# Optimization experiments

Measured on AMD Instinct MI355X. Metric: run time of the kernel, lower is better.

The kernel has to match this reference:

```python
import jax, jax.numpy as jnp
import numpy as np

H = 16      # num_heads
HD = 128    # head_dim = embed_dim // num_heads
BS = 64     # NSA block_size
SEL = 8     # selected blocks per query (block_counts)
WIN = 64    # sliding window (left) size
BASE = 10000.0


def _rope(t):
    # t: [b, n, h, hd]; rotary LRPE (lrpe_type=1)
    n, hd = t.shape[1], t.shape[-1]
    half = hd // 2
    inv = 1.0 / (BASE ** (jnp.arange(half, dtype=jnp.float32) / half))
    th = jnp.arange(n, dtype=jnp.float32)[:, None] * inv[None, :]  # [n, half]
    cos = jnp.cos(th)[None, :, None, :]
    sin = jnp.sin(th)[None, :, None, :]
    t1, t2 = t[..., :half], t[..., half:]
    return jnp.concatenate([t1 * cos - t2 * sin, t1 * sin + t2 * cos], axis=-1)


def _nsa_forward(x, Wq, Wk, Wv, Wg, Wo):
    b, n, d = x.shape
    nb = n // BS
    scale = HD ** -0.5
    q = (x @ Wq).reshape(b, n, H, HD)
    k = (x @ Wk).reshape(b, n, H, HD)
    v = (x @ Wv).reshape(b, n, H, HD)
    g = jax.nn.sigmoid(x @ Wg)                   # [b, n, 3H]
    g_cmp, g_slc, g_swa = jnp.split(g, 3, axis=-1)
    q = _rope(q)
    k = _rope(k)
    idx = jnp.arange(n)

    # --- compression branch: mean-pooled KV blocks, causal over fully-past blocks
    k_cmp = k.reshape(b, nb, BS, H, HD).mean(axis=2)   # [b, nb, h, hd]
    v_cmp = v.reshape(b, nb, BS, H, HD).mean(axis=2)
    s_cmp = jnp.einsum('bnhd,bmhd->bhnm', q, k_cmp) * scale  # [b, h, n, nb]
    blk_end = (jnp.arange(nb) + 1) * BS - 1
    cmp_mask = idx[:, None] >= blk_end[None, :]        # [n, nb]
    p_cmp = jax.nn.softmax(jnp.where(cmp_mask[None, None], s_cmp, -1e30), axis=-1)
    p_cmp = p_cmp * cmp_mask.any(-1)[None, None, :, None]  # zero rows with no valid block
    o_cmp = jnp.einsum('bhnm,bmhd->bnhd', p_cmp, v_cmp)

    # --- selection branch: top-k blocks by compressed scores, current block forced
    cur_blk = jax.nn.one_hot(idx // BS, nb, dtype=jnp.float32)  # [n, nb]
    imp = p_cmp + 2.0 * cur_blk[None, None]
    sel = jax.lax.top_k(imp, SEL)[1]                   # [b, h, n, SEL]
    blk_sel = jax.nn.one_hot(sel, nb).sum(-2) > 0      # [b, h, n, nb]
    causal = idx[:, None] >= idx[None, :]              # [n, n]
    slc_mask = blk_sel[..., idx // BS] & causal[None, None]  # [b, h, n, n]
    s_full = jnp.einsum('bnhd,bmhd->bhnm', q, k) * scale     # [b, h, n, n]
    p_slc = jax.nn.softmax(jnp.where(slc_mask, s_full, -1e30), axis=-1)
    o_slc = jnp.einsum('bhnm,bmhd->bnhd', p_slc, v)

    swa_mask = causal & (idx[:, None] - idx[None, :] <= WIN)
    p_swa = jax.nn.softmax(jnp.where(swa_mask[None, None], s_full, -1e30), axis=-1)
    o_swa = jnp.einsum('bhnm,bmhd->bnhd', p_swa, v)

    o = (o_cmp * g_cmp[..., None] + o_slc * g_slc[..., None]
         + o_swa * g_swa[..., None])                   # [b, n, h, hd]
    return o.reshape(b, n, H * HD) @ Wo


def setup_inputs() -> dict:
    key = jax.random.key(0)
    ks = jax.random.split(key, 6)
    B, N, D = 2, 1024, 2048
    std = 0.02
    return {
        'x': jax.random.normal(ks[0], (B, N, D), jnp.float32),
        'Wq': jax.random.normal(ks[1], (D, H * HD), jnp.float32) * std,
        'Wk': jax.random.normal(ks[2], (D, H * HD), jnp.float32) * std,
        'Wv': jax.random.normal(ks[3], (D, H * HD), jnp.float32) * std,
        'Wg': jax.random.normal(ks[4], (D, 3 * H), jnp.float32) * std,
        'Wo': jax.random.normal(ks[5], (H * HD, D), jnp.float32) * std,
    }


def reference(x, Wq, Wk, Wv, Wg, Wo):
    return _nsa_forward(x, Wq, Wk, Wv, Wg, Wo)
```

## Files before the change

kernel.cpp:

```cpp
#include <hip/hip_runtime.h>
#include <hip/hip_bf16.h>

#define HN   16
#define HDIM 128
#define NSEQ 1024
#define NBLK 16
#define BSZ  64
#define SCALE 0.08838834764831845f
#define QKV_STR 6400
#define KOFS 2048
#define VOFS 4096
#define GOFS 6144

typedef __attribute__((ext_vector_type(8))) short bfrag;
typedef __attribute__((ext_vector_type(4))) float facc;

__device__ __forceinline__ float bf2f(short s) {
  union { unsigned u; float f; } cv;
  cv.u = ((unsigned)(unsigned short)s) << 16;
  return cv.f;
}
__device__ __forceinline__ short f2bf(float f) {
  unsigned u = __float_as_uint(f);
  u = (u + 0x7fff + ((u >> 16) & 1)) >> 16;
  return (short)u;
}

#define ASYNC16(gp, lp)                                                    \
  __builtin_amdgcn_global_load_lds(                                        \
      (const __attribute__((address_space(1))) void*)(gp),                 \
      (__attribute__((address_space(3))) void*)(lp), 16, 0, 0)

#define MFMA16(a, b, c) __builtin_amdgcn_mfma_f32_16x16x32_bf16(a, b, c, 0, 0, 0)

__global__ __launch_bounds__(256) void prep(const float* __restrict__ Wq,
                                            const float* __restrict__ Wk,
                                            const float* __restrict__ Wv,
                                            const float* __restrict__ Wg,
                                            const float* __restrict__ x,
                                            short* __restrict__ w_t,
                                            short* __restrict__ x_bf) {
  __shared__ float tile[32][33];
  const int z = blockIdx.z;
  const int bx = blockIdx.x * 32, by = blockIdx.y * 32;
  const int tx = threadIdx.x & 31, ty = threadIdx.x >> 5;
  if (z == 4) {
#pragma unroll
    for (int i = 0; i < 4; ++i) {
      const int row = by + ty + 8 * i;
      x_bf[(size_t)row * 2048 + bx + tx] = f2bf(x[(size_t)row * 2048 + bx + tx]);
    }
    return;
  }
  if (z == 3) {
    if (blockIdx.x >= 4) return;
#pragma unroll
    for (int i = 0; i < 4; ++i) {
      const int c = bx + tx;
      tile[ty + 8 * i][tx] = (c < 48) ? Wg[(size_t)(by + ty + 8 * i) * 48 + c] : 0.f;
    }
    __syncthreads();
#pragma unroll
    for (int i = 0; i < 4; ++i)
      w_t[(size_t)(GOFS + bx + ty + 8 * i) * 2048 + by + tx] = f2bf(tile[tx][ty + 8 * i]);
    return;
  }
  const float* src = (z == 0) ? Wq : (z == 1) ? Wk : Wv;
#pragma unroll
  for (int i = 0; i < 4; ++i)
    tile[ty + 8 * i][tx] = src[(size_t)(by + ty + 8 * i) * 2048 + bx + tx];
  __syncthreads();
#pragma unroll
  for (int i = 0; i < 4; ++i)
    w_t[(size_t)(z * 2048 + bx + ty + 8 * i) * 2048 + by + tx] = f2bf(tile[tx][ty + 8 * i]);
}

__global__ __launch_bounds__(256) void transpose_cast(const float* __restrict__ src,
                                                      short* __restrict__ dst) {
  __shared__ float tile[32][33];
  const int bx = blockIdx.x * 32, by = blockIdx.y * 32;
  const int tx = threadIdx.x & 31, ty = threadIdx.x >> 5;
#pragma unroll
  for (int i = 0; i < 4; ++i)
    tile[ty + 8 * i][tx] = src[(size_t)(by + ty + 8 * i) * 2048 + bx + tx];
  __syncthreads();
#pragma unroll
  for (int i = 0; i < 4; ++i)
    dst[(size_t)(bx + ty + 8 * i) * 2048 + by + tx] = f2bf(tile[tx][ty + 8 * i]);
}

__global__ __launch_bounds__(512, 1) void gemm256(const short* __restrict__ A,
                                                  const short* __restrict__ Bt,
                                                  short* __restrict__ C,
                                                  int M, int N, int K) {
  __shared__ short lds[2][2][16384];
  const int t = threadIdx.x;
  const int l = t & 63, w = t >> 6;
  const int wm = w >> 2, wn = w & 3;
  const int lm = l & 15, hi = l >> 4;
  const int lanexor = (lm & 7) << 3;
  const int kk0 = (hi * 8) ^ lanexor;
  const int L = blockIdx.x;
  const int row0 = (L & 7) * 256, col0 = (L >> 3) * 256;
  const int nt = K >> 6;

  const int srow = t >> 3;
  const int scol = 8 * ((t & 7) ^ (srow & 7));
  const short* Ab = A + (size_t)(row0 + srow) * K + scol;
  const short* Bb = Bt + (size_t)(col0 + srow) * K + scol;

#define STAGE(mat, srcbase, h, tau, buf)                                     \
  {                                                                          \
    const short* g_ = (srcbase) + (size_t)(h) * 128 * K + (size_t)(tau) * 64;\
    short* d_ = &lds[buf][mat][(h) * 8192 + t * 8];                          \
    ASYNC16(g_, d_);                                                         \
    ASYNC16(g_ + (size_t)64 * K, d_ + 4096);                                 \
  }

  facc acc[8][4] = {};
  bfrag af[8], bf0[4], bf1[4];

  STAGE(0, Ab, 0, 0, 0); STAGE(0, Ab, 1, 0, 0);
  STAGE(1, Bb, 0, 0, 0); STAGE(1, Bb, 1, 0, 0);
  STAGE(1, Bb, 0, 1, 1); STAGE(1, Bb, 1, 1, 1);
  asm volatile("s_waitcnt vmcnt(4)" ::: "memory");
  __builtin_amdgcn_s_barrier();

  for (int tau = 0; tau < nt; ++tau) {
    const int c = tau & 1;
    const int tA = (tau + 1 < nt) ? tau + 1 : nt - 1;
    const int tB = (tau + 2 < nt) ? tau + 2 : nt - 1;

#define DS_A(qm)                                                             \
  _Pragma("unroll") for (int ii = 0; ii < 4; ++ii) {                         \
    const int row_ = wm * 128 + (qm) * 64 + ii * 16 + lm;                    \
    af[ii * 2 + 0] = *(const bfrag*)&lds[c][0][row_ * 64 + kk0];             \
    af[ii * 2 + 1] = *(const bfrag*)&lds[c][0][row_ * 64 + (kk0 ^ 32)];      \
  }
#define DS_B(qn, arr)                                                        \
  _Pragma("unroll") for (int jj = 0; jj < 2; ++jj) {                         \
    const int row_ = wn * 64 + (qn) * 32 + jj * 16 + lm;                     \
    arr[jj * 2 + 0] = *(const bfrag*)&lds[c][1][row_ * 64 + kk0];            \
    arr[jj * 2 + 1] = *(const bfrag*)&lds[c][1][row_ * 64 + (kk0 ^ 32)];     \
  }
#define QUAD(qm, qn, arr)                                                    \
  _Pragma("unroll") for (int ii = 0; ii < 4; ++ii)                           \
  _Pragma("unroll") for (int jj = 0; jj < 2; ++jj) {                         \
    acc[(qm)*4+ii][(qn)*2+jj] = MFMA16(af[ii*2+0], arr[jj*2+0], acc[(qm)*4+ii][(qn)*2+jj]); \
    acc[(qm)*4+ii][(qn)*2+jj] = MFMA16(af[ii*2+1], arr[jj*2+1], acc[(qm)*4+ii][(qn)*2+jj]); \
  }

    DS_A(0); DS_B(0, bf0);
    STAGE(0, Ab, 0, tA, c ^ 1);
    __builtin_amdgcn_s_barrier();
    asm volatile("s_waitcnt lgkmcnt(0)" ::: "memory");
    __builtin_amdgcn_sched_barrier(0);
    __builtin_amdgcn_s_setprio(1);
    QUAD(0, 0, bf0);
    __builtin_amdgcn_s_setprio(0);
    __builtin_amdgcn_s_barrier();

    DS_B(1, bf1);
    STAGE(0, Ab, 1, tA, c ^ 1);
    __builtin_amdgcn_s_barrier();
    asm volatile("s_waitcnt lgkmcnt(0)" ::: "memory");
    __builtin_amdgcn_sched_barrier(0);
    __builtin_amdgcn_s_setprio(1);
    QUAD(0, 1, bf1);
    __builtin_amdgcn_s_setprio(0);
    __builtin_amdgcn_s_barrier();

    DS_A(1);
    STAGE(1, Bb, 0, tB, c);
    __builtin_amdgcn_s_barrier();
    asm volatile("s_waitcnt lgkmcnt(0)" ::: "memory");
    __builtin_amdgcn_sched_barrier(0);
    __builtin_amdgcn_s_setprio(1);
    QUAD(1, 1, bf1);
    __builtin_amdgcn_s_setprio(0);
    __builtin_amdgcn_s_barrier();

    STAGE(1, Bb, 1, tB, c);
    __builtin_amdgcn_s_setprio(1);
    QUAD(1, 0, bf0);
    __builtin_amdgcn_s_setprio(0);
    asm volatile("s_waitcnt vmcnt(4)" ::: "memory");
    __builtin_amdgcn_s_barrier();
  }

#pragma unroll
  for (int i = 0; i < 8; ++i)
#pragma unroll
    for (int j = 0; j < 4; ++j)
#pragma unroll
      for (int rr = 0; rr < 4; ++rr)
        C[(size_t)(row0 + wm * 128 + i * 16 + hi * 4 + rr) * N +
          col0 + wn * 64 + j * 16 + lm] = f2bf(acc[i][j][rr]);
#undef STAGE
#undef DS_A
#undef DS_B
#undef QUAD
}

__device__ __forceinline__ void store_c(float* p, float v) { *p = v; }
__device__ __forceinline__ void store_c(short* p, float v) { *p = f2bf(v); }

template <typename OT>
__global__ __launch_bounds__(256) void gemm_bf16_bt(const short* __restrict__ A,
                                                    const short* __restrict__ Bt,
                                                    OT* __restrict__ C,
                                                    int M, int N, int K) {
  __shared__ short As[128 * 32];
  __shared__ short Bs[128 * 32];
  const int t = threadIdx.x;
  const int l = t & 63, w = t >> 6;
  const int wr = w >> 1, wc = w & 1;
  const int nwg = gridDim.x;
  const int L = blockIdx.x;
  const int wg = (L & 7) * (nwg >> 3) + (L >> 3);
  const int nrow = M >> 7;
  const int row0 = (wg % nrow) * 128, col0 = (wg / nrow) * 128;
  facc acc[4][4] = {};

  const int sr = t >> 2;
  const int sk = (t & 3) * 8;
  const short* Ag0 = A + (size_t)(row0 + sr) * K + sk;
  const short* Ag1 = Ag0 + (size_t)64 * K;
  const short* Bg0 = Bt + (size_t)(col0 + sr) * K + sk;
  const short* Bg1 = Bg0 + (size_t)64 * K;
  short* la = As + t * 8;
  short* lb = Bs + t * 8;

  const int lm = l & 15;
  const int lk = (l >> 4) * 8;

  for (int k0 = 0; k0 < K; k0 += 32) {
    ASYNC16(Ag0 + k0, la);
    ASYNC16(Ag1 + k0, la + 2048);
    ASYNC16(Bg0 + k0, lb);
    ASYNC16(Bg1 + k0, lb + 2048);
    __syncthreads();
    bfrag af[4], bf[4];
#pragma unroll
    for (int i = 0; i < 4; ++i)
      af[i] = *(const bfrag*)&As[(wr * 64 + i * 16 + lm) * 32 + lk];
#pragma unroll
    for (int j = 0; j < 4; ++j)
      bf[j] = *(const bfrag*)&Bs[(wc * 64 + j * 16 + lm) * 32 + lk];
#pragma unroll
    for (int i = 0; i < 4; ++i)
#pragma unroll
      for (int j = 0; j < 4; ++j)
        acc[i][j] = MFMA16(af[i], bf[j], acc[i][j]);
    __syncthreads();
  }

  const int orow = row0 + wr * 64 + (l >> 4) * 4;
  const int ocol = col0 + wc * 64 + lm;
#pragma unroll
  for (int i = 0; i < 4; ++i)
#pragma unroll
    for (int j = 0; j < 4; ++j)
#pragma unroll
      for (int rr = 0; rr < 4; ++rr)
        store_c(&C[(size_t)(orow + i * 16 + rr) * N + ocol + j * 16], acc[i][j][rr]);
}

__global__ __launch_bounds__(256) void rope_tbl(float2* __restrict__ tbl) {
  int i = blockIdx.x * 256 + threadIdx.x;
  int d = i & 63, n = i >> 6;
  float inv = expf(-(float)d * (9.210340371976184f / 64.0f));
  float sn, cs;
  sincosf((float)n * inv, &sn, &cs);
  tbl[i] = make_float2(cs, sn);
}

__global__ __launch_bounds__(256) void rope_qk(short* __restrict__ qkv,
                                               const float2* __restrict__ tbl) {
  int i = blockIdx.x * 256 + threadIdx.x;
  int c = i & 7;
  int h = (i >> 3) & 15;
  int qk = (i >> 7) & 1;
  int n = (i >> 8) & 1023;
  int b = i >> 18;
  short* base = qkv + (size_t)(b * NSEQ + n) * QKV_STR + qk * KOFS + h * HDIM + c * 8;
  const float2* tp = tbl + n * 64 + c * 8;
  bfrag t1 = *(const bfrag*)base, t2 = *(const bfrag*)(base + 64);
  bfrag o1, o2;
#pragma unroll
  for (int j = 0; j < 8; ++j) {
    float2 cssn = tp[j];
    float a = bf2f(t1[j]), bb = bf2f(t2[j]);
    o1[j] = f2bf(a * cssn.x - bb * cssn.y);
    o2[j] = f2bf(a * cssn.y + bb * cssn.x);
  }
  *(bfrag*)base = o1;
  *(bfrag*)(base + 64) = o2;
}

__global__ __launch_bounds__(256) void block_mean(const short* __restrict__ src,
                                                  float* __restrict__ dst) {
  int i = blockIdx.x * 256 + threadIdx.x;
  int d = i & 127;
  int h = (i >> 7) & 15;
  int m = (i >> 11) & 15;
  int b = i >> 15;
  const short* p = src + (size_t)(b * NSEQ + m * BSZ) * QKV_STR + h * HDIM + d;
  float acc = 0.f;
#pragma unroll 8
  for (int j = 0; j < 64; ++j) acc += bf2f(p[(size_t)j * QKV_STR]);
  dst[i] = acc * (1.0f / 64.0f);
}

__global__ __launch_bounds__(256) void v_transpose(const short* __restrict__ qkv,
                                                   short* __restrict__ vt,
                                                   short* __restrict__ vct) {
  __shared__ short tile[64][136];
  const int n0 = blockIdx.x * 64;
  const int h = blockIdx.y, b = blockIdx.z;
  const int t = threadIdx.x;
#pragma unroll
  for (int it = 0; it < 4; ++it) {
    int idx = t + 256 * it;
    int row = idx >> 4, ch = idx & 15;
    *(bfrag*)&tile[row][ch * 8] =
        *(const bfrag*)&qkv[(size_t)(b * NSEQ + n0 + row) * QKV_STR + VOFS + h * HDIM + ch * 8];
  }
  __syncthreads();
#pragma unroll
  for (int it = 0; it < 4; ++it) {
    int idx = t + 256 * it;
    int d = idx >> 3, ch = idx & 7;
    bfrag tv;
    float s = 0.f;
#pragma unroll
    for (int j = 0; j < 8; ++j) {
      tv[j] = tile[ch * 8 + j][d];
      s += bf2f(tv[j]);
    }
    *(bfrag*)&vt[(((size_t)(b * HN + h) * 128) + d) * 1024 + n0 + ch * 8] = tv;
    s += __shfl_down(s, 4);
    s += __shfl_down(s, 2);
    s += __shfl_down(s, 1);
    if ((t & 7) == 0)
      vct[(((size_t)(b * HN + h) * 128) + d) * 16 + (n0 >> 6)] = f2bf(s * (1.0f / 64.0f));
  }
}

__global__ __launch_bounds__(256) void cmp_sel(const short* __restrict__ qkv,
                                               const float* __restrict__ kc,
                                               short* __restrict__ pc,
                                               int* __restrict__ sel) {
  int i = blockIdx.x * 256 + threadIdx.x;
  int n = i & 1023;
  int h = (i >> 10) & 15;
  int b = i >> 14;
  const short* qp = qkv + (size_t)(b * NSEQ + n) * QKV_STR + h * HDIM;
  float qf[HDIM];
#pragma unroll
  for (int d0 = 0; d0 < HDIM; d0 += 8) {
    bfrag qv = *(const bfrag*)&qp[d0];
#pragma unroll
    for (int dd = 0; dd < 8; ++dd) qf[d0 + dd] = bf2f(qv[dd]);
  }
  const int nv = (n + 1) >> 6;
  float s[NBLK];
  float mx = -1e30f;
  for (int m = 0; m < nv; ++m) {
    const float* kp = kc + ((size_t)((b * NBLK + m) * HN + h) << 7);
    float dot = 0.f;
    for (int d = 0; d < HDIM; d += 4) {
      const float4 kv = *(const float4*)&kp[d];
      dot += qf[d] * kv.x + qf[d + 1] * kv.y + qf[d + 2] * kv.z + qf[d + 3] * kv.w;
    }
    s[m] = dot * SCALE;
    mx = fmaxf(mx, s[m]);
  }
  float den = 0.f;
  for (int m = 0; m < nv; ++m) { s[m] = __expf(s[m] - mx); den += s[m]; }
  const float rden = (nv > 0) ? 1.0f / den : 0.f;
  float p[NBLK];
#pragma unroll
  for (int m = 0; m < NBLK; ++m) p[m] = (m < nv) ? s[m] * rden : 0.f;
  bfrag o0, o1;
#pragma unroll
  for (int m = 0; m < 8; ++m) { o0[m] = f2bf(p[m]); o1[m] = f2bf(p[m + 8]); }
  bfrag* pout = (bfrag*)(pc + (size_t)i * 16);
  pout[0] = o0; pout[1] = o1;
  p[n >> 6] += 2.0f;
  int mask = 0;
#pragma unroll
  for (int ss = 0; ss < 8; ++ss) {
    int best = 0;
    float bv = -1e30f;
#pragma unroll
    for (int m = 0; m < NBLK; ++m)
      if (p[m] > bv) { bv = p[m]; best = m; }
    mask |= 1 << best;
    p[best] = -1e30f;
  }
  sel[i] = mask;
}

__global__ __launch_bounds__(64, 2) void attn_mfma(
    const short* __restrict__ qkv, const short* __restrict__ vt,
    const short* __restrict__ vct, const short* __restrict__ pc,
    const int* __restrict__ sel, short* __restrict__ o) {
  const int fid = blockIdx.x;
  const int xcd = fid & 7;
  const int idx = fid >> 3;
  const int pair = (xcd << 2) | (idx & 3);
  const int rt = 63 - (idx >> 2);
  const int h = pair & 15, b = pair >> 4;

  const int l = threadIdx.x;
  const int lm = l & 15, hi = l >> 4;
  const int nbase = rt * 16;

  __shared__ short p_slc[1024];
  __shared__ short p_swa[1024];

  const short* qrow = qkv + (size_t)(b * NSEQ + nbase + lm) * QKV_STR + h * HDIM;
  bfrag qf[4];
#pragma unroll
  for (int ks = 0; ks < 4; ++ks) qf[ks] = *(const bfrag*)&qrow[32 * ks + 8 * hi];

  int selrow = sel[(size_t)(b * HN + h) * NSEQ + nbase + lm];
  int uni = selrow;
#pragma unroll
  for (int m = 1; m < 16; m <<= 1) uni |= __shfl_xor(uni, m);
  int sel4[4];
#pragma unroll
  for (int rg = 0; rg < 4; ++rg) sel4[rg] = __shfl(selrow, 4 * hi + rg);

  const int thi = nbase >> 6;
  const int tlo = (nbase >= 64) ? ((nbase - 64) >> 6) : 0;
  const int wmask = (int)((2u << thi) - (1u << tlo));
  const unsigned am = (unsigned)(uni | wmask) & (unsigned)((2u << thi) - 1);

  facc acc_slc[8] = {}, acc_swa[8] = {};
  float ps_s[4] = {0.f, 0.f, 0.f, 0.f}, ps_w[4] = {0.f, 0.f, 0.f, 0.f};

  const short* kbase0 = qkv + (size_t)(b * NSEQ) * QKV_STR + KOFS + h * HDIM + 8 * hi;
  const short* vtb0 = vt + ((size_t)(b * HN + h) * 128) * 1024 + 8 * hi;

  int ct = __ffs((int)am) - 1;
  bfrag ka0, ka1, ka2, ka3;
  {
    const short* kr = kbase0 + (size_t)(ct * 64 + lm) * QKV_STR;
    ka0 = *(const bfrag*)(kr);
    ka1 = *(const bfrag*)(kr + 32);
    ka2 = *(const bfrag*)(kr + 64);
    ka3 = *(const bfrag*)(kr + 96);
  }

  while (ct >= 0) {
    const unsigned rem = am & ~((2u << ct) - 1);
    const int nct = rem ? (__ffs((int)rem) - 1) : -1;
    const bool do_s = (uni >> ct) & 1;
    const bool do_w = (wmask >> ct) & 1;

    facc sacc[4] = {};
#pragma unroll
    for (int f = 0; f < 4; ++f) {
      const int pct = (f < 3) ? ct : (nct >= 0 ? nct : ct);
      const int pfr = (f < 3) ? 16 * (f + 1) : 0;
      const short* krn = kbase0 + (size_t)(pct * 64 + pfr + lm) * QKV_STR;
      bfrag kn0 = *(const bfrag*)(krn);
      bfrag kn1 = *(const bfrag*)(krn + 32);
      bfrag kn2 = *(const bfrag*)(krn + 64);
      bfrag kn3 = *(const bfrag*)(krn + 96);
      sacc[f] = MFMA16(qf[0], ka0, sacc[f]);
      sacc[f] = MFMA16(qf[1], ka1, sacc[f]);
      sacc[f] = MFMA16(qf[2], ka2, sacc[f]);
      sacc[f] = MFMA16(qf[3], ka3, sacc[f]);
      ka0 = kn0; ka1 = kn1; ka2 = kn2; ka3 = kn3;
    }

    const short* vtb = vtb0 + ct * 64;
    bfrag vb0[8];
#pragma unroll
    for (int df = 0; df < 8; ++df)
      vb0[df] = *(const bfrag*)&vtb[(size_t)(16 * df + lm) * 1024];

#pragma unroll
    for (int f = 0; f < 4; ++f) {
      const int col = ct * 64 + 16 * f + lm;
#pragma unroll
      for (int rg = 0; rg < 4; ++rg) {
        const int row = nbase + 4 * hi + rg;
        float e = __expf(sacc[f][rg] * SCALE);
        e = (col <= row) ? e : 0.f;
        float es = ((sel4[rg] >> ct) & 1) ? e : 0.f;
        float ew = (row - col <= 64) ? e : 0.f;
        ps_s[rg] += es;
        ps_w[rg] += ew;
        const int srow = 4 * hi + rg;
        const int sidx = (64 * srow + 16 * f + lm) ^ ((srow & 7) << 3);
        if (do_s) p_slc[sidx] = f2bf(es);
        if (do_w) p_swa[sidx] = f2bf(ew);
      }
    }
    __syncthreads();

    {
      const int ridx0 = (64 * lm + 8 * hi) ^ ((lm & 7) << 3);
      bfrag pas = {}, paw = {};
      if (do_s) pas = *(const bfrag*)&p_slc[ridx0];
      if (do_w) paw = *(const bfrag*)&p_swa[ridx0];
      bfrag vb1[8];
#pragma unroll
      for (int df = 0; df < 8; ++df)
        vb1[df] = *(const bfrag*)&vtb[(size_t)(16 * df + lm) * 1024 + 32];
#pragma unroll
      for (int df = 0; df < 8; ++df) {
        if (do_s) acc_slc[df] = MFMA16(pas, vb0[df], acc_slc[df]);
        if (do_w) acc_swa[df] = MFMA16(paw, vb0[df], acc_swa[df]);
      }
      const int ridx1 = (64 * lm + 8 * hi + 32) ^ ((lm & 7) << 3);
      bfrag pas1 = {}, paw1 = {};
      if (do_s) pas1 = *(const bfrag*)&p_slc[ridx1];
      if (do_w) paw1 = *(const bfrag*)&p_swa[ridx1];
#pragma unroll
      for (int df = 0; df < 8; ++df) {
        if (do_s) acc_slc[df] = MFMA16(pas1, vb1[df], acc_slc[df]);
        if (do_w) acc_swa[df] = MFMA16(paw1, vb1[df], acc_swa[df]);
      }
    }
    __syncthreads();
    ct = nct;
  }

  facc acc_cmp[8] = {};
  {
    bfrag pa = {};
    if (hi < 2)
      pa = *(const bfrag*)&pc[((size_t)(b * HN + h) * NSEQ + nbase + lm) * 16 + 8 * hi];
#pragma unroll
    for (int df = 0; df < 8; ++df) {
      bfrag vb = {};
      if (hi < 2)
        vb = *(const bfrag*)&vct[(((size_t)(b * HN + h) * 128) + 16 * df + lm) * 16 + 8 * hi];
      acc_cmp[df] = MFMA16(pa, vb, acc_cmp[df]);
    }
  }

#pragma unroll
  for (int m = 1; m < 16; m <<= 1) {
#pragma unroll
    for (int rg = 0; rg < 4; ++rg) {
      ps_s[rg] += __shfl_xor(ps_s[rg], m);
      ps_w[rg] += __shfl_xor(ps_w[rg], m);
    }
  }

  float inv_s[4], inv_w[4], gcv[4], gsv[4], gwv[4];
#pragma unroll
  for (int rg = 0; rg < 4; ++rg) {
    inv_s[rg] = 1.0f / ps_s[rg];
    inv_w[rg] = 1.0f / ps_w[rg];
    const short* gp = qkv + (size_t)(b * NSEQ + nbase + 4 * hi + rg) * QKV_STR + GOFS;
    gcv[rg] = 1.0f / (1.0f + __expf(-bf2f(gp[h])));
    gsv[rg] = 1.0f / (1.0f + __expf(-bf2f(gp[16 + h])));
    gwv[rg] = 1.0f / (1.0f + __expf(-bf2f(gp[32 + h])));
  }

  short* obase = o + (size_t)(b * NSEQ + nbase) * 2048 + h * HDIM;
#pragma unroll
  for (int df = 0; df < 8; ++df)
#pragma unroll
    for (int rg = 0; rg < 4; ++rg) {
      float val = gcv[rg] * acc_cmp[df][rg] +
                  gsv[rg] * acc_slc[df][rg] * inv_s[rg] +
                  gwv[rg] * acc_swa[df][rg] * inv_w[rg];
      obase[(size_t)(4 * hi + rg) * 2048 + 16 * df + lm] = f2bf(val);
    }
}

extern "C" void kernel_launch(void* const* d_in, const int* in_sizes, int n_in,
                              void* d_out, int out_size, void* d_ws, size_t ws_size,
                              hipStream_t stream) {
  const float* x  = (const float*)d_in[0];
  const float* Wq = (const float*)d_in[1];
  const float* Wk = (const float*)d_in[2];
  const float* Wv = (const float*)d_in[3];
  const float* Wg = (const float*)d_in[4];
  const float* Wo = (const float*)d_in[5];
  float* out = (float*)d_out;

  char* w = (char*)d_ws;
  short* x_bf = (short*)w;
  short* o_bf = x_bf;
  w += (size_t)2048 * 2048 * 2;
  short* w_t  = (short*)w;
  w += (size_t)6400 * 2048 * 2;
  short* qkv  = (short*)w;
  w += (size_t)2048 * 6400 * 2;
  float* kc   = (float*)w; w += (size_t)65536 * 4;
  short* vct  = (short*)w; w += (size_t)65536 * 2;
  short* pcb  = (short*)w; w += (size_t)524288 * 2;
  int*   sel  = (int*)w;   w += (size_t)32768 * 4;
  short* vt   = (short*)w; w += (size_t)4194304 * 2;
  float2* tbl = (float2*)w; w += (size_t)65536 * 8;

  const dim3 blk(256);
  prep<<<dim3(64, 64, 5), blk, 0, stream>>>(Wq, Wk, Wv, Wg, x, w_t, x_bf);
  rope_tbl<<<256, blk, 0, stream>>>(tbl);
  gemm256<<<200, dim3(512), 0, stream>>>(x_bf, w_t, qkv, 2048, 6400, 2048);
  rope_qk<<<2048, blk, 0, stream>>>(qkv, tbl);
  block_mean<<<256, blk, 0, stream>>>(qkv + KOFS, kc);
  v_transpose<<<dim3(16, 16, 2), blk, 0, stream>>>(qkv, vt, vct);
  cmp_sel<<<128, blk, 0, stream>>>(qkv, kc, pcb, sel);
  transpose_cast<<<dim3(64, 64), blk, 0, stream>>>(Wo, w_t);
  attn_mfma<<<2048, dim3(64), 0, stream>>>(qkv, vt, vct, pcb, sel, o_bf);
  gemm_bf16_bt<float><<<256, blk, 0, stream>>>(o_bf, w_t, out, 2048, 2048, 2048);
}
```

Measured before the change: 260.5 us.

## Split attention key tiles across two waves, fold rope table into prep, reshape cmp_sel

The attention kernel now runs two wavefronts per block. Each wave handles alternating active key tiles with its own LDS probability buffers, so the per-tile block-wide barriers go away, and the partial accumulators and row sums are reduced through LDS at the end. The rope table generation moves into the prep kernel as an extra z-slice, which saves one launch. cmp_sel switches to 64-thread blocks and accumulates dot products chunk by chunk instead of holding a 128-float q array, which lowers register pressure and raises the block count. The trade-off is extra LDS reduction traffic and barriers, plus possible load imbalance between the two waves.

```diff
diff --git a/kernel.cpp b/kernel.cpp
--- a/kernel.cpp
+++ b/kernel.cpp
@@ -39,11 +39,22 @@
                                             const float* __restrict__ Wg,
                                             const float* __restrict__ x,
                                             short* __restrict__ w_t,
-                                            short* __restrict__ x_bf) {
+                                            short* __restrict__ x_bf,
+                                            float2* __restrict__ tbl) {
   __shared__ float tile[32][33];
   const int z = blockIdx.z;
   const int bx = blockIdx.x * 32, by = blockIdx.y * 32;
   const int tx = threadIdx.x & 31, ty = threadIdx.x >> 5;
+  if (z == 5) {
+    if (blockIdx.y >= 4) return;
+    int i = (blockIdx.y * 64 + blockIdx.x) * 256 + threadIdx.x;
+    int d = i & 63, n = i >> 6;
+    float inv = expf(-(float)d * (9.210340371976184f / 64.0f));
+    float sn, cs;
+    sincosf((float)n * inv, &sn, &cs);
+    tbl[i] = make_float2(cs, sn);
+    return;
+  }
   if (z == 4) {
 #pragma unroll
     for (int i = 0; i < 4; ++i) {
@@ -266,15 +277,6 @@
         store_c(&C[(size_t)(orow + i * 16 + rr) * N + ocol + j * 16], acc[i][j][rr]);
 }
 
-__global__ __launch_bounds__(256) void rope_tbl(float2* __restrict__ tbl) {
-  int i = blockIdx.x * 256 + threadIdx.x;
-  int d = i & 63, n = i >> 6;
-  float inv = expf(-(float)d * (9.210340371976184f / 64.0f));
-  float sn, cs;
-  sincosf((float)n * inv, &sn, &cs);
-  tbl[i] = make_float2(cs, sn);
-}
-
 __global__ __launch_bounds__(256) void rope_qk(short* __restrict__ qkv,
                                                const float2* __restrict__ tbl) {
   int i = blockIdx.x * 256 + threadIdx.x;
@@ -347,35 +349,33 @@
   }
 }
 
-__global__ __launch_bounds__(256) void cmp_sel(const short* __restrict__ qkv,
-                                               const float* __restrict__ kc,
-                                               short* __restrict__ pc,
-                                               int* __restrict__ sel) {
-  int i = blockIdx.x * 256 + threadIdx.x;
+__global__ __launch_bounds__(64) void cmp_sel(const short* __restrict__ qkv,
+                                              const float* __restrict__ kc,
+                                              short* __restrict__ pc,
+                                              int* __restrict__ sel) {
+  int i = blockIdx.x * 64 + threadIdx.x;
   int n = i & 1023;
   int h = (i >> 10) & 15;
   int b = i >> 14;
   const short* qp = qkv + (size_t)(b * NSEQ + n) * QKV_STR + h * HDIM;
-  float qf[HDIM];
-#pragma unroll
+  const int nv = (n + 1) >> 6;
+  float s[NBLK];
+#pragma unroll
+  for (int m = 0; m < NBLK; ++m) s[m] = 0.f;
   for (int d0 = 0; d0 < HDIM; d0 += 8) {
     bfrag qv = *(const bfrag*)&qp[d0];
-#pragma unroll
-    for (int dd = 0; dd < 8; ++dd) qf[d0 + dd] = bf2f(qv[dd]);
-  }
-  const int nv = (n + 1) >> 6;
-  float s[NBLK];
+    float qf[8];
+#pragma unroll
+    for (int dd = 0; dd < 8; ++dd) qf[dd] = bf2f(qv[dd]);
+    for (int m = 0; m < nv; ++m) {
+      const float4* kp = (const float4*)(kc + ((size_t)((b * NBLK + m) * HN + h) << 7) + d0);
+      const float4 k0 = kp[0], k1 = kp[1];
+      s[m] += qf[0] * k0.x + qf[1] * k0.y + qf[2] * k0.z + qf[3] * k0.w +
+              qf[4] * k1.x + qf[5] * k1.y + qf[6] * k1.z + qf[7] * k1.w;
+    }
+  }
   float mx = -1e30f;
-  for (int m = 0; m < nv; ++m) {
-    const float* kp = kc + ((size_t)((b * NBLK + m) * HN + h) << 7);
-    float dot = 0.f;
-    for (int d = 0; d < HDIM; d += 4) {
-      const float4 kv = *(const float4*)&kp[d];
-      dot += qf[d] * kv.x + qf[d + 1] * kv.y + qf[d + 2] * kv.z + qf[d + 3] * kv.w;
-    }
-    s[m] = dot * SCALE;
-    mx = fmaxf(mx, s[m]);
-  }
+  for (int m = 0; m < nv; ++m) { s[m] *= SCALE; mx = fmaxf(mx, s[m]); }
   float den = 0.f;
   for (int m = 0; m < nv; ++m) { s[m] = __expf(s[m] - mx); den += s[m]; }
   const float rden = (nv > 0) ? 1.0f / den : 0.f;
@@ -402,7 +402,7 @@
   sel[i] = mask;
 }
 
-__global__ __launch_bounds__(64, 2) void attn_mfma(
+__global__ __launch_bounds__(128, 4) void attn_mfma(
     const short* __restrict__ qkv, const short* __restrict__ vt,
     const short* __restrict__ vct, const short* __restrict__ pc,
     const int* __restrict__ sel, short* __restrict__ o) {
@@ -413,12 +413,14 @@
   const int rt = 63 - (idx >> 2);
   const int h = pair & 15, b = pair >> 4;
 
-  const int l = threadIdx.x;
+  const int tid = threadIdx.x;
+  const int wid = tid >> 6;
+  const int l = tid & 63;
   const int lm = l & 15, hi = l >> 4;
   const int nbase = rt * 16;
 
-  __shared__ short p_slc[1024];
-  __shared__ short p_swa[1024];
+  __shared__ short pbuf[2][2][1024];
+  float* cb = (float*)&pbuf[0][0][0];
 
   const short* qrow = qkv + (size_t)(b * NSEQ + nbase + lm) * QKV_STR + h * HDIM;
   bfrag qf[4];
@@ -438,15 +440,30 @@
   const int wmask = (int)((2u << thi) - (1u << tlo));
   const unsigned am = (unsigned)(uni | wmask) & (unsigned)((2u << thi) - 1);
 
+  unsigned amw = 0;
+  {
+    unsigned mm = am;
+    int p = 0;
+    while (mm) {
+      unsigned lb = mm & (0u - mm);
+      if ((p & 1) == wid) amw |= lb;
+      mm ^= lb;
+      ++p;
+    }
+  }
+
   facc acc_slc[8] = {}, acc_swa[8] = {};
   float ps_s[4] = {0.f, 0.f, 0.f, 0.f}, ps_w[4] = {0.f, 0.f, 0.f, 0.f};
 
   const short* kbase0 = qkv + (size_t)(b * NSEQ) * QKV_STR + KOFS + h * HDIM + 8 * hi;
   const short* vtb0 = vt + ((size_t)(b * HN + h) * 128) * 1024 + 8 * hi;
-
-  int ct = __ffs((int)am) - 1;
+  short* p_slc = &pbuf[wid][0][0];
+  short* p_swa = &pbuf[wid][1][0];
+
+  int ct = -1;
   bfrag ka0, ka1, ka2, ka3;
-  {
+  if (amw) {
+    ct = __ffs((int)amw) - 1;
     const short* kr = kbase0 + (size_t)(ct * 64 + lm) * QKV_STR;
     ka0 = *(const bfrag*)(kr);
     ka1 = *(const bfrag*)(kr + 32);
@@ -455,7 +472,7 @@
   }
 
   while (ct >= 0) {
-    const unsigned rem = am & ~((2u << ct) - 1);
+    const unsigned rem = amw & ~((2u << ct) - 1);
     const int nct = rem ? (__ffs((int)rem) - 1) : -1;
     const bool do_s = (uni >> ct) & 1;
     const bool do_w = (wmask >> ct) & 1;
@@ -501,7 +518,6 @@
         if (do_w) p_swa[sidx] = f2bf(ew);
       }
     }
-    __syncthreads();
 
     {
       const int ridx0 = (64 * lm + 8 * hi) ^ ((lm & 7) << 3);
@@ -527,8 +543,53 @@
         if (do_w) acc_swa[df] = MFMA16(paw1, vb1[df], acc_swa[df]);
       }
     }
-    __syncthreads();
     ct = nct;
+  }
+
+  __syncthreads();
+  if (wid == 1) {
+    float* q = cb + l * 8;
+#pragma unroll
+    for (int rg = 0; rg < 4; ++rg) { q[rg] = ps_s[rg]; q[4 + rg] = ps_w[rg]; }
+  }
+  __syncthreads();
+  if (wid == 0) {
+    const float* q = cb + l * 8;
+#pragma unroll
+    for (int rg = 0; rg < 4; ++rg) { ps_s[rg] += q[rg]; ps_w[rg] += q[4 + rg]; }
+  }
+  __syncthreads();
+  if (wid == 1) {
+    float* q = cb + l * 32;
+#pragma unroll
+    for (int df = 0; df < 8; ++df)
+#pragma unroll
+      for (int rg = 0; rg < 4; ++rg) q[df * 4 + rg] = acc_slc[df][rg];
+  }
+  __syncthreads();
+  if (wid == 0) {
+    const float* q = cb + l * 32;
+#pragma unroll
+    for (int df = 0; df < 8; ++df)
+#pragma unroll
+      for (int rg = 0; rg < 4; ++rg) acc_slc[df][rg] += q[df * 4 + rg];
+  }
+  __syncthreads();
+  if (wid == 1) {
+    float* q = cb + l * 32;
+#pragma unroll
+    for (int df = 0; df < 8; ++df)
+#pragma unroll
+      for (int rg = 0; rg < 4; ++rg) q[df * 4 + rg] = acc_swa[df][rg];
+  }
+  __syncthreads();
+  if (wid != 0) return;
+  {
+    const float* q = cb + l * 32;
+#pragma unroll
+    for (int df = 0; df < 8; ++df)
+#pragma unroll
+      for (int rg = 0; rg < 4; ++rg) acc_swa[df][rg] += q[df * 4 + rg];
   }
 
   facc acc_cmp[8] = {};
@@ -604,14 +665,13 @@
   float2* tbl = (float2*)w; w += (size_t)65536 * 8;
 
   const dim3 blk(256);
-  prep<<<dim3(64, 64, 5), blk, 0, stream>>>(Wq, Wk, Wv, Wg, x, w_t, x_bf);
-  rope_tbl<<<256, blk, 0, stream>>>(tbl);
+  prep<<<dim3(64, 64, 6), blk, 0, stream>>>(Wq, Wk, Wv, Wg, x, w_t, x_bf, tbl);
   gemm256<<<200, dim3(512), 0, stream>>>(x_bf, w_t, qkv, 2048, 6400, 2048);
   rope_qk<<<2048, blk, 0, stream>>>(qkv, tbl);
   block_mean<<<256, blk, 0, stream>>>(qkv + KOFS, kc);
   v_transpose<<<dim3(16, 16, 2), blk, 0, stream>>>(qkv, vt, vct);
-  cmp_sel<<<128, blk, 0, stream>>>(qkv, kc, pcb, sel);
+  cmp_sel<<<512, dim3(64), 0, stream>>>(qkv, kc, pcb, sel);
   transpose_cast<<<dim3(64, 64), blk, 0, stream>>>(Wo, w_t);
-  attn_mfma<<<2048, dim3(64), 0, stream>>>(qkv, vt, vct, pcb, sel, o_bf);
+  attn_mfma<<<2048, dim3(128), 0, stream>>>(qkv, vt, vct, pcb, sel, o_bf);
   gemm_bf16_bt<float><<<256, blk, 0, stream>>>(o_bf, w_t, out, 2048, 2048, 2048);
 }
```

Measured after the change: 442.3 us. 1.7x slower.

## Split attention head dim across blocks, fold rope table into prep, reshape cmp_sel

Applied to the files above, without the earlier changes.

The attention kernel now launches twice as many single-wave blocks, each computing half of the 128-wide head dimension, so accumulator registers halve and occupancy is raised to 4 waves per SIMD. This also drops the two __syncthreads per tile, which should be safe for a single-wave block. The rope table computation moves into an extra z-slice of the prep kernel to save a launch, and cmp_sel switches to 64-thread blocks with a streaming dot product that no longer keeps a 128-float q array in registers. Splitting the head dimension means the QK scores and softmax are computed twice per row tile, duplicating that work.

```diff
diff --git a/kernel.cpp b/kernel.cpp
--- a/kernel.cpp
+++ b/kernel.cpp
@@ -39,11 +39,22 @@
                                             const float* __restrict__ Wg,
                                             const float* __restrict__ x,
                                             short* __restrict__ w_t,
-                                            short* __restrict__ x_bf) {
+                                            short* __restrict__ x_bf,
+                                            float2* __restrict__ tbl) {
   __shared__ float tile[32][33];
   const int z = blockIdx.z;
   const int bx = blockIdx.x * 32, by = blockIdx.y * 32;
   const int tx = threadIdx.x & 31, ty = threadIdx.x >> 5;
+  if (z == 5) {
+    if (blockIdx.y >= 4) return;
+    int i = (blockIdx.y * 64 + blockIdx.x) * 256 + threadIdx.x;
+    int d = i & 63, n = i >> 6;
+    float inv = expf(-(float)d * (9.210340371976184f / 64.0f));
+    float sn, cs;
+    sincosf((float)n * inv, &sn, &cs);
+    tbl[i] = make_float2(cs, sn);
+    return;
+  }
   if (z == 4) {
 #pragma unroll
     for (int i = 0; i < 4; ++i) {
@@ -266,15 +277,6 @@
         store_c(&C[(size_t)(orow + i * 16 + rr) * N + ocol + j * 16], acc[i][j][rr]);
 }
 
-__global__ __launch_bounds__(256) void rope_tbl(float2* __restrict__ tbl) {
-  int i = blockIdx.x * 256 + threadIdx.x;
-  int d = i & 63, n = i >> 6;
-  float inv = expf(-(float)d * (9.210340371976184f / 64.0f));
-  float sn, cs;
-  sincosf((float)n * inv, &sn, &cs);
-  tbl[i] = make_float2(cs, sn);
-}
-
 __global__ __launch_bounds__(256) void rope_qk(short* __restrict__ qkv,
                                                const float2* __restrict__ tbl) {
   int i = blockIdx.x * 256 + threadIdx.x;
@@ -347,35 +349,33 @@
   }
 }
 
-__global__ __launch_bounds__(256) void cmp_sel(const short* __restrict__ qkv,
-                                               const float* __restrict__ kc,
-                                               short* __restrict__ pc,
-                                               int* __restrict__ sel) {
-  int i = blockIdx.x * 256 + threadIdx.x;
+__global__ __launch_bounds__(64) void cmp_sel(const short* __restrict__ qkv,
+                                              const float* __restrict__ kc,
+                                              short* __restrict__ pc,
+                                              int* __restrict__ sel) {
+  int i = blockIdx.x * 64 + threadIdx.x;
   int n = i & 1023;
   int h = (i >> 10) & 15;
   int b = i >> 14;
   const short* qp = qkv + (size_t)(b * NSEQ + n) * QKV_STR + h * HDIM;
-  float qf[HDIM];
-#pragma unroll
+  const int nv = (n + 1) >> 6;
+  float s[NBLK];
+#pragma unroll
+  for (int m = 0; m < NBLK; ++m) s[m] = 0.f;
   for (int d0 = 0; d0 < HDIM; d0 += 8) {
     bfrag qv = *(const bfrag*)&qp[d0];
-#pragma unroll
-    for (int dd = 0; dd < 8; ++dd) qf[d0 + dd] = bf2f(qv[dd]);
-  }
-  const int nv = (n + 1) >> 6;
-  float s[NBLK];
+    float qf[8];
+#pragma unroll
+    for (int dd = 0; dd < 8; ++dd) qf[dd] = bf2f(qv[dd]);
+    for (int m = 0; m < nv; ++m) {
+      const float4* kp = (const float4*)(kc + ((size_t)((b * NBLK + m) * HN + h) << 7) + d0);
+      const float4 k0 = kp[0], k1 = kp[1];
+      s[m] += qf[0] * k0.x + qf[1] * k0.y + qf[2] * k0.z + qf[3] * k0.w +
+              qf[4] * k1.x + qf[5] * k1.y + qf[6] * k1.z + qf[7] * k1.w;
+    }
+  }
   float mx = -1e30f;
-  for (int m = 0; m < nv; ++m) {
-    const float* kp = kc + ((size_t)((b * NBLK + m) * HN + h) << 7);
-    float dot = 0.f;
-    for (int d = 0; d < HDIM; d += 4) {
-      const float4 kv = *(const float4*)&kp[d];
-      dot += qf[d] * kv.x + qf[d + 1] * kv.y + qf[d + 2] * kv.z + qf[d + 3] * kv.w;
-    }
-    s[m] = dot * SCALE;
-    mx = fmaxf(mx, s[m]);
-  }
+  for (int m = 0; m < nv; ++m) { s[m] *= SCALE; mx = fmaxf(mx, s[m]); }
   float den = 0.f;
   for (int m = 0; m < nv; ++m) { s[m] = __expf(s[m] - mx); den += s[m]; }
   const float rden = (nv > 0) ? 1.0f / den : 0.f;
@@ -402,7 +402,7 @@
   sel[i] = mask;
 }
 
-__global__ __launch_bounds__(64, 2) void attn_mfma(
+__global__ __launch_bounds__(64, 4) void attn_mfma(
     const short* __restrict__ qkv, const short* __restrict__ vt,
     const short* __restrict__ vct, const short* __restrict__ pc,
     const int* __restrict__ sel, short* __restrict__ o) {
@@ -410,12 +410,14 @@
   const int xcd = fid & 7;
   const int idx = fid >> 3;
   const int pair = (xcd << 2) | (idx & 3);
-  const int rt = 63 - (idx >> 2);
+  const int half = (idx >> 2) & 1;
+  const int rt = 63 - (idx >> 3);
   const int h = pair & 15, b = pair >> 4;
 
   const int l = threadIdx.x;
   const int lm = l & 15, hi = l >> 4;
   const int nbase = rt * 16;
+  const int dofs = half * 64;
 
   __shared__ short p_slc[1024];
   __shared__ short p_swa[1024];
@@ -438,11 +440,11 @@
   const int wmask = (int)((2u << thi) - (1u << tlo));
   const unsigned am = (unsigned)(uni | wmask) & (unsigned)((2u << thi) - 1);
 
-  facc acc_slc[8] = {}, acc_swa[8] = {};
+  facc acc_slc[4] = {}, acc_swa[4] = {};
   float ps_s[4] = {0.f, 0.f, 0.f, 0.f}, ps_w[4] = {0.f, 0.f, 0.f, 0.f};
 
   const short* kbase0 = qkv + (size_t)(b * NSEQ) * QKV_STR + KOFS + h * HDIM + 8 * hi;
-  const short* vtb0 = vt + ((size_t)(b * HN + h) * 128) * 1024 + 8 * hi;
+  const short* vtb0 = vt + ((size_t)(b * HN + h) * 128 + dofs) * 1024 + 8 * hi;
 
   int ct = __ffs((int)am) - 1;
   bfrag ka0, ka1, ka2, ka3;
@@ -478,9 +480,9 @@
     }
 
     const short* vtb = vtb0 + ct * 64;
-    bfrag vb0[8];
-#pragma unroll
-    for (int df = 0; df < 8; ++df)
+    bfrag vb0[4];
+#pragma unroll
+    for (int df = 0; df < 4; ++df)
       vb0[df] = *(const bfrag*)&vtb[(size_t)(16 * df + lm) * 1024];
 
 #pragma unroll
@@ -501,19 +503,18 @@
         if (do_w) p_swa[sidx] = f2bf(ew);
       }
     }
-    __syncthreads();
 
     {
       const int ridx0 = (64 * lm + 8 * hi) ^ ((lm & 7) << 3);
       bfrag pas = {}, paw = {};
       if (do_s) pas = *(const bfrag*)&p_slc[ridx0];
       if (do_w) paw = *(const bfrag*)&p_swa[ridx0];
-      bfrag vb1[8];
-#pragma unroll
-      for (int df = 0; df < 8; ++df)
+      bfrag vb1[4];
+#pragma unroll
+      for (int df = 0; df < 4; ++df)
         vb1[df] = *(const bfrag*)&vtb[(size_t)(16 * df + lm) * 1024 + 32];
 #pragma unroll
-      for (int df = 0; df < 8; ++df) {
+      for (int df = 0; df < 4; ++df) {
         if (do_s) acc_slc[df] = MFMA16(pas, vb0[df], acc_slc[df]);
         if (do_w) acc_swa[df] = MFMA16(paw, vb0[df], acc_swa[df]);
       }
@@ -522,25 +523,24 @@
       if (do_s) pas1 = *(const bfrag*)&p_slc[ridx1];
       if (do_w) paw1 = *(const bfrag*)&p_swa[ridx1];
 #pragma unroll
-      for (int df = 0; df < 8; ++df) {
+      for (int df = 0; df < 4; ++df) {
         if (do_s) acc_slc[df] = MFMA16(pas1, vb1[df], acc_slc[df]);
         if (do_w) acc_swa[df] = MFMA16(paw1, vb1[df], acc_swa[df]);
       }
     }
-    __syncthreads();
     ct = nct;
   }
 
-  facc acc_cmp[8] = {};
+  facc acc_cmp[4] = {};
   {
     bfrag pa = {};
     if (hi < 2)
       pa = *(const bfrag*)&pc[((size_t)(b * HN + h) * NSEQ + nbase + lm) * 16 + 8 * hi];
 #pragma unroll
-    for (int df = 0; df < 8; ++df) {
+    for (int df = 0; df < 4; ++df) {
       bfrag vb = {};
       if (hi < 2)
-        vb = *(const bfrag*)&vct[(((size_t)(b * HN + h) * 128) + 16 * df + lm) * 16 + 8 * hi];
+        vb = *(const bfrag*)&vct[(((size_t)(b * HN + h) * 128) + dofs + 16 * df + lm) * 16 + 8 * hi];
       acc_cmp[df] = MFMA16(pa, vb, acc_cmp[df]);
     }
   }
@@ -565,9 +565,9 @@
     gwv[rg] = 1.0f / (1.0f + __expf(-bf2f(gp[32 + h])));
   }
 
-  short* obase = o + (size_t)(b * NSEQ + nbase) * 2048 + h * HDIM;
-#pragma unroll
-  for (int df = 0; df < 8; ++df)
+  short* obase = o + (size_t)(b * NSEQ + nbase) * 2048 + h * HDIM + dofs;
+#pragma unroll
+  for (int df = 0; df < 4; ++df)
 #pragma unroll
     for (int rg = 0; rg < 4; ++rg) {
       float val = gcv[rg] * acc_cmp[df][rg] +
@@ -604,14 +604,13 @@
   float2* tbl = (float2*)w; w += (size_t)65536 * 8;
 
   const dim3 blk(256);
-  prep<<<dim3(64, 64, 5), blk, 0, stream>>>(Wq, Wk, Wv, Wg, x, w_t, x_bf);
-  rope_tbl<<<256, blk, 0, stream>>>(tbl);
+  prep<<<dim3(64, 64, 6), blk, 0, stream>>>(Wq, Wk, Wv, Wg, x, w_t, x_bf, tbl);
   gemm256<<<200, dim3(512), 0, stream>>>(x_bf, w_t, qkv, 2048, 6400, 2048);
   rope_qk<<<2048, blk, 0, stream>>>(qkv, tbl);
   block_mean<<<256, blk, 0, stream>>>(qkv + KOFS, kc);
   v_transpose<<<dim3(16, 16, 2), blk, 0, stream>>>(qkv, vt, vct);
-  cmp_sel<<<128, blk, 0, stream>>>(qkv, kc, pcb, sel);
+  cmp_sel<<<512, dim3(64), 0, stream>>>(qkv, kc, pcb, sel);
   transpose_cast<<<dim3(64, 64), blk, 0, stream>>>(Wo, w_t);
-  attn_mfma<<<2048, dim3(64), 0, stream>>>(qkv, vt, vct, pcb, sel, o_bf);
+  attn_mfma<<<4096, dim3(64), 0, stream>>>(qkv, vt, vct, pcb, sel, o_bf);
   gemm_bf16_bt<float><<<256, blk, 0, stream>>>(o_bf, w_t, out, 2048, 2048, 2048);
 }
```

After: 411.6 us. 58.0% more time.
